# Performance work log

Measured on AMD Instinct MI355X. Metric: run time of the kernel, lower is better.

Reference implementation:

```python
import jax, jax.numpy as jnp
import numpy as np

B, T, H, L, V, M = 512, 64, 450, 56, 780, 8
S = T * B + 2  # slot 0 = zero padding vector, slots 1..T*B = edges, slot S-1 = dummy sink


def setup_inputs() -> dict:
    key = jax.random.key(0)
    ks = jax.random.split(key, 20)
    g = lambda i, shape, scale=0.05: jax.random.normal(ks[i], shape, jnp.float32) * scale
    return dict(
        tree_vecs=jax.random.normal(ks[0], (B, L), jnp.float32),
        x_wid=jax.random.randint(ks[1], (T, B), 0, V),
        pred_wid=jax.random.randint(ks[2], (T, B), 0, V),
        root_wid=jax.random.randint(ks[3], (B,), 0, V),
        h_nei_idx=jax.random.randint(ks[4], (T, B, M), 0, T * B + 1),
        o_nei_idx=jax.random.randint(ks[5], (T, B, M), 0, T * B + 1),
        root_o_nei_idx=jax.random.randint(ks[6], (B, M), 0, T * B + 1),
        valid=jax.random.randint(ks[7], (T, B), 0, 2),
        direction=jax.random.randint(ks[8], (T, B), 0, 2),
        emb=g(9, (V, H), 1.0),
        Wz=g(10, (H, 2 * H)), bz=jnp.zeros((H,), jnp.float32),
        Wr=g(11, (H, H)), br=jnp.zeros((H,), jnp.float32),
        Ur=g(12, (H, H)),
        Wh=g(13, (H, 2 * H)), bh=jnp.zeros((H,), jnp.float32),
        W=g(14, (H, L + H)), bW=jnp.zeros((H,), jnp.float32),
        U=g(15, (H, L + 2 * H)), bU=jnp.zeros((H,), jnp.float32),
        Wo=g(16, (V, H)), bWo=jnp.zeros((V,), jnp.float32),
        Us=g(17, (1, H)), bUs=jnp.zeros((1,), jnp.float32),
    )


def _gru(x, h_nei, Wz, bz, Wr, br, Ur, Wh, bh):
    # x: [N,H], h_nei: [N,M,H]  (JTNN tree GRU)
    sum_h = h_nei.sum(1)
    z = jax.nn.sigmoid(jnp.concatenate([x, sum_h], 1) @ Wz.T + bz)
    r = jax.nn.sigmoid((x @ Wr.T + br)[:, None, :] + h_nei @ Ur.T)
    gated = (r * h_nei).sum(1)
    h_tilde = jnp.tanh(jnp.concatenate([x, gated], 1) @ Wh.T + bh)
    return (1.0 - z) * sum_h + z * h_tilde


def reference(tree_vecs, x_wid, pred_wid, root_wid, h_nei_idx, o_nei_idx,
              root_o_nei_idx, valid, direction, emb, Wz, bz, Wr, br, Ur,
              Wh, bh, W, bW, U, bU, Wo, bWo, Us, bUs):
    xe_all = emb[x_wid]                              # [T,B,H]
    validf = valid.astype(jnp.float32)
    slots = jnp.arange(B)

    def step(h_buf, inputs):
        t, xe, h_idx, o_idx, v = inputs
        h_nei = h_buf[h_idx]                         # [B,M,H] gather (excl. real_y)
        new_h = _gru(xe, h_nei, Wz, bz, Wr, br, Ur, Wh, bh)
        cur_o = h_buf[o_idx].sum(1)                  # [B,H] sum-pool all neighbors
        slot = jnp.where(v > 0, 1 + t * B + slots, S - 1)
        h_buf = h_buf.at[slot].set(jnp.where(v[:, None] > 0, new_h, 0.0))
        return h_buf, (new_h, cur_o)

    h0 = jnp.zeros((S, H), jnp.float32)
    h_buf, (new_h_all, cur_o_all) = jax.lax.scan(
        step, h0, (jnp.arange(T), xe_all, h_nei_idx, o_nei_idx, valid))

    tv_rep = jnp.broadcast_to(tree_vecs, (T, B, L)).reshape(T * B, L)

    # ---- label (pred) loss: root rows + timestep rows where direction==1 ----
    pred_mask = jnp.concatenate([jnp.ones((B,), jnp.float32),
                                 (validf * direction.astype(jnp.float32)).reshape(-1)])
    pred_hidden = jnp.concatenate([jnp.zeros((B, H), jnp.float32),
                                   new_h_all.reshape(T * B, H)], 0)
    pred_tv = jnp.concatenate([tree_vecs, tv_rep], 0)
    pred_tgt = jnp.concatenate([root_wid, pred_wid.reshape(-1)])
    pv = jax.nn.relu(jnp.concatenate([pred_hidden, pred_tv], 1) @ W.T + bW)
    scores = pv @ Wo.T + bWo                         # [(T+1)*B, V]
    ll = jax.nn.log_softmax(scores, -1)
    ce = -jnp.take_along_axis(ll, pred_tgt[:, None], 1)[:, 0]
    pred_loss = (ce * pred_mask).sum() / B
    pred_acc = (((jnp.argmax(scores, 1) == pred_tgt).astype(jnp.float32)
                 * pred_mask).sum() / pred_mask.sum())

    # ---- topological (stop) loss: timestep rows + final root rows ----
    root_o = h_buf[root_o_nei_idx].sum(1)            # [B,H]
    stop_hidden = jnp.concatenate([
        jnp.concatenate([xe_all.reshape(T * B, H), cur_o_all.reshape(T * B, H), tv_rep], 1),
        jnp.concatenate([emb[root_wid], root_o, tree_vecs], 1)], 0)
    smask = jnp.concatenate([validf.reshape(-1), jnp.ones((B,), jnp.float32)])
    stgt = jnp.concatenate([direction.astype(jnp.float32).reshape(-1),
                            jnp.zeros((B,), jnp.float32)])
    sv = jax.nn.relu(stop_hidden @ U.T + bU)
    ss = (sv @ Us.T + bUs)[:, 0]
    bce = jnp.maximum(ss, 0.0) - ss * stgt + jnp.log1p(jnp.exp(-jnp.abs(ss)))
    stop_loss = (bce * smask).sum() / B
    stops = (ss >= 0).astype(jnp.float32)
    stop_acc = (((stops == stgt).astype(jnp.float32) * smask).sum() / smask.sum())

    return pred_loss, stop_loss, pred_acc, stop_acc
```

## Files before the change

### kernel.cpp

```cpp
#include <hip/hip_runtime.h>
#include <math.h>

#define Bq 512
#define Tq 64
#define Hq 450
#define Lq 56
#define Vq 780
#define Mq 8
#define TBq 32768
#define Sq 32770
#define HP 480
#define NPB 130
#define NPCAP 12288
#define NSCAP 20480
#define CH2 6144
#define NCH2 2

using bf16x8 = __attribute__((ext_vector_type(8))) __bf16;
using f32x4  = __attribute__((ext_vector_type(4))) float;
using u32x4  = __attribute__((ext_vector_type(4))) unsigned;

__device__ __forceinline__ ushort f2bf(float f){
    union { float f; unsigned u; } c; c.f = f;
    unsigned u = c.u;
    return (ushort)((u + 0x7FFFu + ((u >> 16) & 1u)) >> 16);
}
__device__ __forceinline__ float bf2f(ushort h){
    union { unsigned u; float f; } c; c.u = ((unsigned)h) << 16;
    return c.f;
}
__device__ __forceinline__ unsigned pk2(float a, float b){
    return (unsigned)f2bf(a) | ((unsigned)f2bf(b) << 16);
}
__device__ __forceinline__ float sigmf(float x){
    return __builtin_amdgcn_rcpf(1.f + __expf(-x));
}
__device__ __forceinline__ float tanhfast(float x){
    float e2 = __expf(2.f * x);
    return 1.f - 2.f * __builtin_amdgcn_rcpf(e2 + 1.f);
}

__global__ void convAll_k(
    const float* __restrict__ emb, const float* __restrict__ tree,
    const float* __restrict__ Wz, const float* __restrict__ Wr,
    const float* __restrict__ Ur, const float* __restrict__ Wh,
    const float* __restrict__ Wm, const float* __restrict__ U, const float* __restrict__ Wo,
    ushort* embb, ushort* treeb, ushort* WzX, ushort* WzS, ushort* WrB,
    ushort* WhX, ushort* WhG, ushort* UrB, ushort* WHp, ushort* UXp,
    ushort* UOp, ushort* WOp, ushort* WLp, ushort* ULp)
{
    int job = blockIdx.y, n = blockIdx.x;
    const float* src; ushort* dst; int Npad, Nsrc, Ksrc, Kpad, len, off;
    switch(job){
      case 0:  src=emb;  dst=embb; Npad=896; Nsrc=780; Ksrc=450; Kpad=480; len=450; off=0;   break;
      case 1:  src=tree; dst=treeb;Npad=512; Nsrc=512; Ksrc=56;  Kpad=64;  len=56;  off=0;   break;
      case 2:  src=Wz;   dst=WzX;  Npad=512; Nsrc=450; Ksrc=900; Kpad=480; len=450; off=0;   break;
      case 3:  src=Wz;   dst=WzS;  Npad=512; Nsrc=450; Ksrc=900; Kpad=480; len=450; off=450; break;
      case 4:  src=Wr;   dst=WrB;  Npad=512; Nsrc=450; Ksrc=450; Kpad=480; len=450; off=0;   break;
      case 5:  src=Wh;   dst=WhX;  Npad=512; Nsrc=450; Ksrc=900; Kpad=480; len=450; off=0;   break;
      case 6:  src=Wh;   dst=WhG;  Npad=512; Nsrc=450; Ksrc=900; Kpad=480; len=450; off=450; break;
      case 7:  src=Ur;   dst=UrB;  Npad=512; Nsrc=450; Ksrc=450; Kpad=480; len=450; off=0;   break;
      case 8:  src=Wm;   dst=WHp;  Npad=512; Nsrc=450; Ksrc=506; Kpad=480; len=450; off=0;   break;
      case 9:  src=U;    dst=UXp;  Npad=512; Nsrc=450; Ksrc=956; Kpad=480; len=450; off=0;   break;
      case 10: src=U;    dst=UOp;  Npad=512; Nsrc=450; Ksrc=956; Kpad=480; len=450; off=450; break;
      case 11: src=Wo;   dst=WOp;  Npad=832; Nsrc=780; Ksrc=450; Kpad=480; len=450; off=0;   break;
      case 12: src=Wm;   dst=WLp;  Npad=512; Nsrc=450; Ksrc=506; Kpad=64;  len=56;  off=450; break;
      default: src=U;    dst=ULp;  Npad=512; Nsrc=450; Ksrc=956; Kpad=64;  len=56;  off=900; break;
    }
    if (n >= Npad) return;
    for (int k = threadIdx.x; k < Kpad; k += blockDim.x){
        float v = 0.f;
        if (n < Nsrc && k < len) v = src[(size_t)n*Ksrc + off + k];
        dst[(size_t)n*Kpad + k] = f2bf(v);
    }
}

template<class APtr>
__device__ __forceinline__ void mgemm2(APtr&& aptr, const ushort* __restrict__ Bw, int ldb,
                                       int KT, int col0, f32x4 acc[4][2])
{
    __shared__ __align__(16) char As[2][128*80];
    __shared__ __align__(16) char Bs[2][64*80];
    const int tid = threadIdx.x;
    const int lane = tid & 63;
    const int w = tid >> 6, wm = w >> 1, wn = w & 1;
    const int ac = (tid & 3) * 8;
    const size_t boff = (size_t)(col0 + (tid >> 2)) * ldb;
    u32x4 ra0, ra1, rb;
    auto ld = [&](int k0){
        ra0 = *(const u32x4*)(aptr(0, k0) + ac);
        ra1 = *(const u32x4*)(aptr(1, k0) + ac);
        rb  = *(const u32x4*)(Bw + boff + k0 + ac);
    };
    const int wr_a0 = (tid>>2)*80 + (tid&3)*16;
    const int wr_a1 = ((tid>>2)+64)*80 + (tid&3)*16;
    const int wr_b  = (tid>>2)*80 + (tid&3)*16;
    const int rd_a  = (wm*64 + (lane&15))*80 + (lane>>4)*16;
    const int rd_b  = (wn*32 + (lane&15))*80 + (lane>>4)*16;
    ld(0);
    *(u32x4*)(As[0]+wr_a0) = ra0; *(u32x4*)(As[0]+wr_a1) = ra1; *(u32x4*)(Bs[0]+wr_b) = rb;
#pragma unroll
    for (int f=0;f<4;f++)
#pragma unroll
        for (int g=0;g<2;g++) acc[f][g] = (f32x4){0.f,0.f,0.f,0.f};
    __syncthreads();
    for (int kt=0; kt<KT; ++kt){
        const int cur = kt & 1;
        if (kt+1 < KT) ld((kt+1)*32);
        bf16x8 bF[2];
#pragma unroll
        for (int g=0; g<2; g++) bF[g] = *(const bf16x8*)(Bs[cur] + rd_b + g*16*80);
#pragma unroll
        for (int f=0; f<4; f++){
            bf16x8 aF = *(const bf16x8*)(As[cur] + rd_a + f*16*80);
#pragma unroll
            for (int g=0; g<2; g++)
                acc[f][g] = __builtin_amdgcn_mfma_f32_16x16x32_bf16(aF, bF[g], acc[f][g], 0, 0, 0);
        }
        if (kt+1 < KT){
            *(u32x4*)(As[cur^1]+wr_a0) = ra0; *(u32x4*)(As[cur^1]+wr_a1) = ra1;
            *(u32x4*)(Bs[cur^1]+wr_b) = rb;
        }
        __syncthreads();
    }
}

#define EPI_PRE  const int lane = threadIdx.x & 63; const int w_ = threadIdx.x >> 6; \
                 const int wm = w_ >> 1, wn = w_ & 1;

__device__ __forceinline__ void pre_body(const ushort* __restrict__ A, int lda,
    const ushort* __restrict__ Bw, const float* __restrict__ bias,
    ushort* __restrict__ out, int Mr, int KT)
{
    const int row0 = blockIdx.y*128, col0 = blockIdx.x*64;
    const int tid = threadIdx.x;
    const ushort* p0 = A + (size_t)(row0 + (tid>>2))*lda;
    const ushort* p1 = p0 + (size_t)64*lda;
    f32x4 acc[4][2];
    mgemm2([&](int which,int k0){ return (which?p1:p0)+k0; }, Bw, lda, KT, col0, acc);
    EPI_PRE
#pragma unroll
    for (int f=0; f<4; f++)
#pragma unroll
      for (int g=0; g<2; g++){
        int col = col0 + wn*32 + g*16 + (lane & 15);
        if (col >= HP) continue;
        float bb = 0.f;
        if (col < Hq && bias) bb = bias[col];
#pragma unroll
        for (int j=0; j<4; j++){
            int row = row0 + wm*64 + f*16 + ((lane>>4)<<2) + j;
            if (row < Mr) out[(size_t)row*HP + col] = (col < Hq) ? f2bf(acc[f][g][j] + bb) : 0;
        }
      }
}

__global__ __launch_bounds__(256) void preE_k(
    const ushort* __restrict__ embb,
    const ushort* __restrict__ WzX, const ushort* __restrict__ WrB,
    const ushort* __restrict__ WhX, const ushort* __restrict__ UXp,
    const float* __restrict__ bz, const float* __restrict__ br,
    const float* __restrict__ bh, const float* __restrict__ bU,
    ushort* __restrict__ EZ, ushort* __restrict__ ER,
    ushort* __restrict__ EH, ushort* __restrict__ EU)
{
    const ushort* Bw; const float* bias; ushort* out;
    switch(blockIdx.z){
      case 0:  Bw=WzX; bias=bz; out=EZ; break;
      case 1:  Bw=WrB; bias=br; out=ER; break;
      case 2:  Bw=WhX; bias=bh; out=EH; break;
      default: Bw=UXp; bias=bU; out=EU; break;
    }
    pre_body(embb, HP, Bw, bias, out, Vq, 15);
}

__global__ __launch_bounds__(256) void preT_k(
    const ushort* __restrict__ treeb,
    const ushort* __restrict__ WLp, const ushort* __restrict__ ULp,
    const float* __restrict__ bW, ushort* __restrict__ TP, ushort* __restrict__ TU)
{
    const ushort* Bw = blockIdx.z ? ULp : WLp;
    const float* bias = blockIdx.z ? nullptr : bW;
    ushort* out = blockIdx.z ? TU : TP;
    pre_body(treeb, 64, Bw, bias, out, Bq, 2);
}

__device__ __forceinline__ bool cmask(int which, int gr,
    const int* __restrict__ valid, const int* __restrict__ dir)
{
    if (which == 0) return (gr < Bq) ? true : (valid[gr-Bq] && dir[gr-Bq]);
    return (gr < TBq) ? (valid[gr] != 0) : true;
}
__global__ void cnt_k(const int* __restrict__ valid, const int* __restrict__ dir,
                      int* __restrict__ cnts)
{
    int which = blockIdx.y;
    int gr = blockIdx.x*256 + threadIdx.x;
    bool m = cmask(which, gr, valid, dir);
    unsigned long long bal = __ballot(m);
    if ((threadIdx.x & 63) == 0)
        atomicAdd(&cnts[which*NPB + blockIdx.x], (int)__popcll(bal));
}
__global__ void scan_k(const int* __restrict__ cnts, int* __restrict__ offs,
                       int* __restrict__ totals)
{
    if (threadIdx.x == 0){
        int a = 0;
        for (int i=0;i<NPB;i++){ offs[i] = a; a += cnts[i]; }
        totals[0] = a;
        int b = 0;
        for (int i=0;i<NPB;i++){ offs[NPB+i] = b; b += cnts[NPB+i]; }
        totals[1] = b;
    }
}
__global__ void fill_k(const int* __restrict__ valid, const int* __restrict__ dir,
                       const int* __restrict__ offs, int* __restrict__ listp,
                       int* __restrict__ lists)
{
    __shared__ int woff[4];
    int which = blockIdx.y;
    int gr = blockIdx.x*256 + threadIdx.x;
    bool m = cmask(which, gr, valid, dir);
    unsigned long long bal = __ballot(m);
    int lane = threadIdx.x & 63, wv = threadIdx.x >> 6;
    if (lane == 0) woff[wv] = (int)__popcll(bal);
    __syncthreads();
    int prev = 0;
    for (int i=0;i<wv;i++) prev += woff[i];
    if (m){
        int rank = prev + (int)__popcll(bal & ((1ull << lane) - 1ull));
        int pos = offs[which*NPB + blockIdx.x] + rank;
        if (which == 0){ if (pos < NPCAP) listp[pos] = gr; }
        else           { if (pos < NSCAP) lists[pos] = gr; }
    }
}

__global__ void vfill_k(const int* __restrict__ valid,
                        int* __restrict__ vcnt, int* __restrict__ vlist)
{
    __shared__ int woff[8];
    const int t = blockIdx.x;
    const int b = threadIdx.x;
    bool m = valid[t*Bq + b] != 0;
    unsigned long long bal = __ballot(m);
    int lane = b & 63, wv = b >> 6;
    if (lane == 0) woff[wv] = (int)__popcll(bal);
    __syncthreads();
    int prev = 0;
    for (int i=0;i<wv;i++) prev += woff[i];
    if (m) vlist[t*Bq + prev + (int)__popcll(bal & ((1ull<<lane)-1ull))] = b;
    if (threadIdx.x == 511){
        int tot = 0;
        for (int i=0;i<8;i++) tot += woff[i];
        vcnt[t] = tot;
    }
}

__global__ __launch_bounds__(256) void gather_k(int t,
    const int* __restrict__ x_wid, const int* __restrict__ h_nei_idx,
    const ushort* __restrict__ ER,
    const int* __restrict__ vcnt, const int* __restrict__ vlist,
    const ushort* __restrict__ hbuf, const ushort* __restrict__ uhbuf,
    ushort* __restrict__ sumhC, ushort* __restrict__ gatedC)
{
    const int cnt = vcnt[t];
    const int task = blockIdx.x*256 + threadIdx.x;
    if (task >= cnt*57) return;
    const int i = task / 57;
    const int c = task - i*57;
    const int j0 = c*8;
    const int b = vlist[t*Bq + i];
    const int base = t*Bq + b;
    const int wid = x_wid[base];
    const int* ip = h_nei_idx + (size_t)base*Mq;
    int idx[Mq];
#pragma unroll
    for (int m=0;m<Mq;m++) idx[m] = ip[m];
    float er[8];
    { u32x4 ev = *(const u32x4*)(ER + (size_t)wid*HP + j0);
#pragma unroll
      for (int e=0;e<8;e++) er[e] = bf2f((ushort)((ev[e>>1] >> ((e&1)*16)) & 0xffff)); }
    float sh[8] = {0,0,0,0,0,0,0,0};
    float gt[8] = {0,0,0,0,0,0,0,0};
#pragma unroll
    for (int m=0;m<Mq;m++){
        u32x4 hv = *(const u32x4*)(hbuf  + (size_t)idx[m]*HP + j0);
        u32x4 uv = *(const u32x4*)(uhbuf + (size_t)idx[m]*HP + j0);
#pragma unroll
        for (int e=0;e<8;e++){
            float h = bf2f((ushort)((hv[e>>1] >> ((e&1)*16)) & 0xffff));
            float u = bf2f((ushort)((uv[e>>1] >> ((e&1)*16)) & 0xffff));
            sh[e] += h;
            gt[e] += h * sigmf(er[e] + u);
        }
    }
    u32x4 so, go;
    so[0]=pk2(sh[0],sh[1]); so[1]=pk2(sh[2],sh[3]);
    so[2]=pk2(sh[4],sh[5]); so[3]=pk2(sh[6],sh[7]);
    go[0]=pk2(gt[0],gt[1]); go[1]=pk2(gt[2],gt[3]);
    go[2]=pk2(gt[4],gt[5]); go[3]=pk2(gt[6],gt[7]);
    *(u32x4*)(sumhC  + (size_t)i*HP + j0) = so;
    *(u32x4*)(gatedC + (size_t)i*HP + j0) = go;
}

__global__ __launch_bounds__(256) void zh_k(int t,
    const int* __restrict__ x_wid,
    const int* __restrict__ vcnt, const int* __restrict__ vlist,
    const ushort* __restrict__ EZ, const ushort* __restrict__ EH,
    const ushort* __restrict__ WzS, const ushort* __restrict__ WhG,
    const ushort* __restrict__ sumhC, const ushort* __restrict__ gatedC,
    ushort* __restrict__ nhC, ushort* __restrict__ hbuf)
{
    const int cnt = vcnt[t];
    const int rows0 = blockIdx.x*32;
    if (rows0 >= cnt) return;
    const int cols0 = blockIdx.y*32;
    const int lane = threadIdx.x & 63, w = threadIdx.x >> 6;
    const int wr = w >> 1, wc = w & 1;
    const int ai = rows0 + wr*16 + (lane & 15);
    const int C  = cols0 + wc*16 + (lane & 15);
    const int kq = (lane >> 4) * 8;
    const ushort* aZp = sumhC  + (size_t)ai*HP + kq;
    const ushort* aGp = gatedC + (size_t)ai*HP + kq;
    const ushort* bZp = WzS + (size_t)C*HP + kq;
    const ushort* bGp = WhG + (size_t)C*HP + kq;
    f32x4 accZ = (f32x4){0,0,0,0}, accH = (f32x4){0,0,0,0};
#pragma unroll 5
    for (int kt=0; kt<15; ++kt){
        const int kb = kt*32;
        bf16x8 aZ = *(const bf16x8*)(aZp + kb);
        bf16x8 aG = *(const bf16x8*)(aGp + kb);
        bf16x8 bZ = *(const bf16x8*)(bZp + kb);
        bf16x8 bG = *(const bf16x8*)(bGp + kb);
        accZ = __builtin_amdgcn_mfma_f32_16x16x32_bf16(aZ, bZ, accZ, 0, 0, 0);
        accH = __builtin_amdgcn_mfma_f32_16x16x32_bf16(aG, bG, accH, 0, 0, 0);
    }
#pragma unroll
    for (int j=0; j<4; j++){
        const int i = rows0 + wr*16 + ((lane>>4)<<2) + j;
        if (i >= cnt) continue;
        const int b = vlist[t*Bq + i];
        const int base = t*Bq + b;
        ushort o = 0;
        if (C < Hq){
            const int wid = x_wid[base];
            float z  = sigmf(accZ[j] + bf2f(EZ[(size_t)wid*HP + C]));
            float ht = tanhfast(accH[j] + bf2f(EH[(size_t)wid*HP + C]));
            float sh = bf2f(sumhC[(size_t)i*HP + C]);
            o = f2bf((1.f - z)*sh + z*ht);
            hbuf[(size_t)(1 + base)*HP + C] = o;
        }
        nhC[(size_t)i*HP + C] = o;
    }
}

__global__ __launch_bounds__(256) void ur_k(int t,
    const int* __restrict__ vcnt, const int* __restrict__ vlist,
    const ushort* __restrict__ UrB, const ushort* __restrict__ nhC,
    ushort* __restrict__ uhbuf)
{
    const int cnt = vcnt[t];
    const int rows0 = blockIdx.x*32;
    if (rows0 >= cnt) return;
    const int cols0 = blockIdx.y*32;
    const int lane = threadIdx.x & 63, w = threadIdx.x >> 6;
    const int wr = w >> 1, wc = w & 1;
    const int ai = rows0 + wr*16 + (lane & 15);
    const int C  = cols0 + wc*16 + (lane & 15);
    const int kq = (lane >> 4) * 8;
    const ushort* aNp = nhC + (size_t)ai*HP + kq;
    const ushort* bUp = UrB + (size_t)C*HP + kq;
    f32x4 acc = (f32x4){0,0,0,0};
#pragma unroll 5
    for (int kt=0; kt<15; ++kt){
        const int kb = kt*32;
        bf16x8 aN = *(const bf16x8*)(aNp + kb);
        bf16x8 bU = *(const bf16x8*)(bUp + kb);
        acc = __builtin_amdgcn_mfma_f32_16x16x32_bf16(aN, bU, acc, 0, 0, 0);
    }
    if (C < Hq){
#pragma unroll
        for (int j=0; j<4; j++){
            const int i = rows0 + wr*16 + ((lane>>4)<<2) + j;
            if (i >= cnt) continue;
            const int b = vlist[t*Bq + i];
            uhbuf[(size_t)(1 + t*Bq + b)*HP + C] = f2bf(acc[j]);
        }
    }
}

__global__ __launch_bounds__(256) void pred1c_k(const int* __restrict__ np_,
    const int* __restrict__ listp, const ushort* __restrict__ hbuf,
    const ushort* __restrict__ TP, const ushort* __restrict__ WHp,
    ushort* __restrict__ pv)
{
    const int np = *np_;
    const int row0 = blockIdx.x*128;
    if (row0 >= np) return;
    const int col0 = blockIdx.y*64;
    const int tid = threadIdx.x;
    int i0 = row0 + (tid>>2), i1 = i0 + 64;
    int g0 = (i0 < np) ? listp[i0] : 0;
    int g1 = (i1 < np) ? listp[i1] : 0;
    const ushort* p0 = (g0 < Bq) ? hbuf : hbuf + (size_t)(1 + g0 - Bq)*HP;
    const ushort* p1 = (g1 < Bq) ? hbuf : hbuf + (size_t)(1 + g1 - Bq)*HP;
    f32x4 acc[4][2];
    mgemm2([&](int which,int k0){ return (which?p1:p0)+k0; }, WHp, HP, 15, col0, acc);
    EPI_PRE
#pragma unroll
    for (int f=0; f<4; f++)
#pragma unroll
      for (int g=0; g<2; g++){
        int col = col0 + wn*32 + g*16 + (lane & 15);
        if (col >= HP) continue;
#pragma unroll
        for (int j=0; j<4; j++){
            int i = row0 + wm*64 + f*16 + ((lane>>4)<<2) + j;
            if (i >= np) continue;
            int gr = listp[i];
            int b = (gr < Bq) ? gr : ((gr - Bq) & (Bq-1));
            float v = 0.f;
            if (col < Hq) v = fmaxf(acc[f][g][j] + bf2f(TP[(size_t)b*HP + col]), 0.f);
            pv[(size_t)i*HP + col] = f2bf(v);
        }
      }
}

__global__ __launch_bounds__(256) void pred2c_k(int cs, const int* __restrict__ np_,
    const ushort* __restrict__ pv, const ushort* __restrict__ WOp,
    const float* __restrict__ bWo, float* __restrict__ scores)
{
    const int np = *np_;
    const int row0 = blockIdx.x*128;
    if (cs + row0 >= np) return;
    const int col0 = blockIdx.y*64;
    const int tid = threadIdx.x;
    const ushort* p0 = pv + (size_t)(cs + row0 + (tid>>2))*HP;
    const ushort* p1 = p0 + (size_t)64*HP;
    f32x4 acc[4][2];
    mgemm2([&](int which,int k0){ return (which?p1:p0)+k0; }, WOp, HP, 15, col0, acc);
    EPI_PRE
#pragma unroll
    for (int f=0; f<4; f++)
#pragma unroll
      for (int g=0; g<2; g++){
        int col = col0 + wn*32 + g*16 + (lane & 15);
        if (col >= Vq) continue;
        float bc = bWo[col];
#pragma unroll
        for (int j=0; j<4; j++){
            int r = row0 + wm*64 + f*16 + ((lane>>4)<<2) + j;
            scores[(size_t)r*832 + col] = acc[f][g][j] + bc;
        }
      }
}

__global__ __launch_bounds__(256) void predred_k(int cs, const int* __restrict__ np_,
    const int* __restrict__ listp, const float* __restrict__ scores,
    const int* __restrict__ pred_wid, const int* __restrict__ root_wid,
    float* __restrict__ accv)
{
    const int np = *np_;
    int nrows = np - cs; if (nrows > CH2) nrows = CH2;
    const int lane = threadIdx.x & 63, wv = threadIdx.x >> 6;
    const int wid_g = blockIdx.x*4 + wv, nw = gridDim.x*4;
    float ce = 0.f, hit = 0.f, cnt = 0.f;
    for (int r = wid_g; r < nrows; r += nw){
        const float* sc = scores + (size_t)r*832;
        int gr = listp[cs + r];
        int tgt = (gr < Bq) ? root_wid[gr] : pred_wid[gr - Bq];
        float vals[13];
        float bv = -INFINITY, tv = 0.f; int bi = 0;
#pragma unroll
        for (int q=0; q<13; q++){
            int j = lane + q*64;
            float v = (j < Vq) ? sc[j] : -INFINITY;
            vals[q] = v;
            if (v > bv){ bv = v; bi = j; }
            if (j == tgt) tv = v;
        }
#pragma unroll
        for (int off=32; off; off>>=1){
            float ov = __shfl_xor(bv, off); int oi = __shfl_xor(bi, off);
            if (ov > bv || (ov == bv && oi < bi)){ bv = ov; bi = oi; }
        }
        float s = 0.f;
#pragma unroll
        for (int q=0; q<13; q++){
            int j = lane + q*64;
            if (j < Vq) s += __expf(vals[q] - bv);
        }
#pragma unroll
        for (int off=32; off; off>>=1) s += __shfl_xor(s, off);
#pragma unroll
        for (int off=32; off; off>>=1) tv += __shfl_xor(tv, off);
        if (lane == 0){
            ce += bv + logf(s) - tv;
            hit += (bi == tgt) ? 1.f : 0.f;
            cnt += 1.f;
        }
    }
    __shared__ float L[3][4];
    if (lane == 0){ L[0][wv] = ce; L[1][wv] = hit; L[2][wv] = cnt; }
    __syncthreads();
    if (threadIdx.x == 0){
        float a = L[0][0]+L[0][1]+L[0][2]+L[0][3];
        float b = L[1][0]+L[1][1]+L[1][2]+L[1][3];
        float c = L[2][0]+L[2][1]+L[2][2]+L[2][3];
        if (c != 0.f){
            atomicAdd(&accv[0], a);
            atomicAdd(&accv[1], b);
            atomicAdd(&accv[2], c);
        }
    }
}

__global__ __launch_bounds__(256) void curo_c(const int* __restrict__ ns_,
    const int* __restrict__ lists,
    const int* __restrict__ o_nei_idx, const int* __restrict__ root_o_nei,
    const ushort* __restrict__ hbuf, ushort* __restrict__ curo)
{
    const int ns = *ns_;
    const int task = blockIdx.x*256 + threadIdx.x;
    if (task >= ns*60) return;
    const int i = task / 60;
    const int c = task - i*60;
    const int j0 = c*8;
    const int gr = lists[i];
    int idx[Mq];
    if (gr < TBq){
        int tt = gr >> 9;
#pragma unroll
        for (int m=0;m<Mq;m++){
            int ix = o_nei_idx[(size_t)gr*Mq + m];
            idx[m] = (ix <= tt*Bq) ? ix : 0;
        }
    } else {
#pragma unroll
        for (int m=0;m<Mq;m++) idx[m] = root_o_nei[(size_t)(gr-TBq)*Mq + m];
    }
    float sh[8] = {0,0,0,0,0,0,0,0};
#pragma unroll
    for (int m=0;m<Mq;m++){
        u32x4 hv = *(const u32x4*)(hbuf + (size_t)idx[m]*HP + j0);
#pragma unroll
        for (int e=0;e<8;e++)
            sh[e] += bf2f((ushort)((hv[e>>1] >> ((e&1)*16)) & 0xffff));
    }
    u32x4 so;
    so[0]=pk2(sh[0],sh[1]); so[1]=pk2(sh[2],sh[3]);
    so[2]=pk2(sh[4],sh[5]); so[3]=pk2(sh[6],sh[7]);
    *(u32x4*)(curo + (size_t)i*HP + j0) = so;
}

__global__ __launch_bounds__(256) void stopc_k(const int* __restrict__ ns_,
    const int* __restrict__ lists, const int* __restrict__ x_wid,
    const int* __restrict__ root_wid, const ushort* __restrict__ curo,
    const ushort* __restrict__ UOp, const ushort* __restrict__ EU,
    const ushort* __restrict__ TU, const float* __restrict__ Usf,
    float* __restrict__ ss)
{
    const int ns = *ns_;
    const int row0 = blockIdx.x*128;
    if (row0 >= ns) return;
    const int col0 = blockIdx.y*64;
    const int tid = threadIdx.x;
    const ushort* p0 = curo + (size_t)(row0 + (tid>>2))*HP;
    const ushort* p1 = p0 + (size_t)64*HP;
    f32x4 acc[4][2];
    mgemm2([&](int which,int k0){ return (which?p1:p0)+k0; }, UOp, HP, 15, col0, acc);
    EPI_PRE
#pragma unroll
    for (int f=0; f<4; f++){
#pragma unroll
        for (int j=0; j<4; j++){
            int i = row0 + wm*64 + f*16 + ((lane>>4)<<2) + j;
            float p = 0.f;
            if (i < ns){
                int gr = lists[i];
                int wid = (gr < TBq) ? x_wid[gr] : root_wid[gr - TBq];
                int b   = (gr < TBq) ? (gr & (Bq-1)) : (gr - TBq);
                const ushort* eu = EU + (size_t)wid*HP;
                const ushort* tu = TU + (size_t)b*HP;
#pragma unroll
                for (int g=0; g<2; g++){
                    int col = col0 + wn*32 + g*16 + (lane & 15);
                    if (col < Hq)
                        p += fmaxf(acc[f][g][j] + bf2f(eu[col]) + bf2f(tu[col]), 0.f) * Usf[col];
                }
            }
            p += __shfl_xor(p, 1); p += __shfl_xor(p, 2);
            p += __shfl_xor(p, 4); p += __shfl_xor(p, 8);
            if ((lane & 15) == 0 && i < ns) atomicAdd(&ss[i], p);
        }
    }
}

__global__ void stopfin_k(const int* __restrict__ ns_, const int* __restrict__ lists,
    const float* __restrict__ ss, const float* __restrict__ bUs,
    const int* __restrict__ direction, float* __restrict__ accv)
{
    const int ns = *ns_;
    int i = blockIdx.x*256 + threadIdx.x;
    float bce = 0.f, hit = 0.f, c = 0.f;
    if (i < ns){
        int gr = lists[i];
        float s = ss[i] + bUs[0];
        float stgt = (gr < TBq) ? (float)direction[gr] : 0.f;
        bce = fmaxf(s,0.f) - s*stgt + log1pf(__expf(-fabsf(s)));
        hit = ((((s >= 0.f) ? 1.f : 0.f) == stgt) ? 1.f : 0.f);
        c = 1.f;
    }
    for (int off=32; off; off>>=1){
        bce += __shfl_down(bce, off);
        hit += __shfl_down(hit, off);
        c   += __shfl_down(c,   off);
    }
    if ((threadIdx.x & 63) == 0 && c != 0.f){
        atomicAdd(&accv[3], bce);
        atomicAdd(&accv[4], hit);
        atomicAdd(&accv[5], c);
    }
}

__global__ void finalize_k(const float* __restrict__ accv, float* __restrict__ out){
    if (threadIdx.x == 0){
        out[0] = accv[0] / (float)Bq;
        out[1] = accv[3] / (float)Bq;
        out[2] = accv[1] / accv[2];
        out[3] = accv[4] / accv[5];
    }
}

extern "C" void kernel_launch(void* const* d_in, const int* in_sizes, int n_in,
                              void* d_out, int out_size, void* d_ws, size_t ws_size,
                              hipStream_t stream) {
    (void)in_sizes; (void)n_in; (void)out_size; (void)ws_size;
    const float* tree_vecs = (const float*)d_in[0];
    const int*   x_wid     = (const int*)d_in[1];
    const int*   pred_wid  = (const int*)d_in[2];
    const int*   root_wid  = (const int*)d_in[3];
    const int*   h_nei_idx = (const int*)d_in[4];
    const int*   o_nei_idx = (const int*)d_in[5];
    const int*   root_o_nei= (const int*)d_in[6];
    const int*   valid     = (const int*)d_in[7];
    const int*   direction = (const int*)d_in[8];
    const float* emb       = (const float*)d_in[9];
    const float* Wz        = (const float*)d_in[10];
    const float* bz        = (const float*)d_in[11];
    const float* Wr        = (const float*)d_in[12];
    const float* br        = (const float*)d_in[13];
    const float* Ur        = (const float*)d_in[14];
    const float* Wh        = (const float*)d_in[15];
    const float* bh        = (const float*)d_in[16];
    const float* Wm        = (const float*)d_in[17];
    const float* bW        = (const float*)d_in[18];
    const float* U         = (const float*)d_in[19];
    const float* bU        = (const float*)d_in[20];
    const float* Wo        = (const float*)d_in[21];
    const float* bWo       = (const float*)d_in[22];
    const float* Us        = (const float*)d_in[23];
    const float* bUs       = (const float*)d_in[24];

    char* w = (char*)d_ws; size_t off = 0;
    auto alloc = [&](size_t bytes)->void*{ void* p = w + off; off += (bytes + 255) & ~(size_t)255; return p; };

    ushort* hbuf  = (ushort*)alloc((size_t)Sq*HP*2);
    ushort* uhbuf = (ushort*)alloc((size_t)Sq*HP*2);
    ushort* embb  = (ushort*)alloc((size_t)896*HP*2);
    ushort* treeb = (ushort*)alloc((size_t)Bq*64*2);
    ushort* WzX   = (ushort*)alloc((size_t)512*HP*2);
    ushort* WzS   = (ushort*)alloc((size_t)512*HP*2);
    ushort* WrB   = (ushort*)alloc((size_t)512*HP*2);
    ushort* WhX   = (ushort*)alloc((size_t)512*HP*2);
    ushort* WhG   = (ushort*)alloc((size_t)512*HP*2);
    ushort* UrB   = (ushort*)alloc((size_t)512*HP*2);
    ushort* WHp   = (ushort*)alloc((size_t)512*HP*2);
    ushort* UXp   = (ushort*)alloc((size_t)512*HP*2);
    ushort* UOp   = (ushort*)alloc((size_t)512*HP*2);
    ushort* WOp   = (ushort*)alloc((size_t)832*HP*2);
    ushort* WLp   = (ushort*)alloc((size_t)512*64*2);
    ushort* ULp   = (ushort*)alloc((size_t)512*64*2);
    ushort* EZ    = (ushort*)alloc((size_t)896*HP*2);
    ushort* ER    = (ushort*)alloc((size_t)896*HP*2);
    ushort* EH    = (ushort*)alloc((size_t)896*HP*2);
    ushort* EU    = (ushort*)alloc((size_t)896*HP*2);
    ushort* TP    = (ushort*)alloc((size_t)Bq*HP*2);
    ushort* TU    = (ushort*)alloc((size_t)Bq*HP*2);
    ushort* sumhC = (ushort*)alloc((size_t)Bq*HP*2);
    ushort* gatedC= (ushort*)alloc((size_t)Bq*HP*2);
    ushort* nhC   = (ushort*)alloc((size_t)Bq*HP*2);
    ushort* pv    = (ushort*)alloc((size_t)NPCAP*HP*2);
    float*  scores= (float*)alloc((size_t)CH2*832*4);
    float*  ss    = (float*)alloc((size_t)NSCAP*4);
    int*    listp = (int*)alloc((size_t)NPCAP*4);
    int*    lists = (int*)alloc((size_t)NSCAP*4);
    int*    vlist = (int*)alloc((size_t)Tq*Bq*4);
    int*    vcnt  = (int*)alloc((size_t)Tq*4);
    int*    meta  = (int*)alloc((size_t)(NPB*4 + 2 + 16)*4);
    int*    cnts  = meta;
    int*    offs  = meta + 2*NPB;
    int*    tot   = meta + 4*NPB;
    float*  accv  = (float*)(meta + 4*NPB + 2);
    ushort* curo  = pv;

    (void)hipMemsetAsync(hbuf,  0, (size_t)Sq*HP*2, stream);
    (void)hipMemsetAsync(uhbuf, 0, (size_t)Sq*HP*2, stream);
    (void)hipMemsetAsync(ss,    0, (size_t)NSCAP*4, stream);
    (void)hipMemsetAsync(meta,  0, (size_t)(NPB*4 + 2 + 16)*4, stream);

    convAll_k<<<dim3(896,14), 128, 0, stream>>>(
        emb, tree_vecs, Wz, Wr, Ur, Wh, Wm, U, Wo,
        embb, treeb, WzX, WzS, WrB, WhX, WhG, UrB, WHp, UXp, UOp, WOp, WLp, ULp);

    preE_k<<<dim3(8,7,4), 256, 0, stream>>>(embb, WzX, WrB, WhX, UXp,
                                            bz, br, bh, bU, EZ, ER, EH, EU);
    preT_k<<<dim3(8,4,2), 256, 0, stream>>>(treeb, WLp, ULp, bW, TP, TU);

    cnt_k <<<dim3(NPB,2), 256, 0, stream>>>(valid, direction, cnts);
    scan_k<<<1, 64, 0, stream>>>(cnts, offs, tot);
    fill_k<<<dim3(NPB,2), 256, 0, stream>>>(valid, direction, offs, listp, lists);
    vfill_k<<<Tq, 512, 0, stream>>>(valid, vcnt, vlist);

    for (int t=0; t<Tq; t++){
        gather_k<<<115, 256, 0, stream>>>(t, x_wid, h_nei_idx, ER, vcnt, vlist,
                                          hbuf, uhbuf, sumhC, gatedC);
        zh_k<<<dim3(16,15), 256, 0, stream>>>(t, x_wid, vcnt, vlist, EZ, EH,
                                              WzS, WhG, sumhC, gatedC, nhC, hbuf);
        ur_k<<<dim3(16,15), 256, 0, stream>>>(t, vcnt, vlist, UrB, nhC, uhbuf);
    }

    pred1c_k<<<dim3(NPCAP/128, 8), 256, 0, stream>>>(tot, listp, hbuf, TP, WHp, pv);
    for (int c=0; c<NCH2; c++){
        int cs = c*CH2;
        pred2c_k<<<dim3(CH2/128, 13), 256, 0, stream>>>(cs, tot, pv, WOp, bWo, scores);
        predred_k<<<256, 256, 0, stream>>>(cs, tot, listp, scores, pred_wid, root_wid, accv);
    }

    curo_c<<<(NSCAP*60 + 255)/256, 256, 0, stream>>>(tot+1, lists, o_nei_idx, root_o_nei, hbuf, curo);
    stopc_k<<<dim3(NSCAP/128, 8), 256, 0, stream>>>(tot+1, lists, x_wid, root_wid,
                                                    curo, UOp, EU, TU, Us, ss);
    stopfin_k<<<NSCAP/256, 256, 0, stream>>>(tot+1, lists, ss, bUs, direction, accv);

    finalize_k<<<1, 64, 0, stream>>>(accv, (float*)d_out);
}
```

Baseline: 1.352 ms.

## Swap MFMA operands to transpose accumulators and vectorize GEMM epilogues

Swaps the A/B operands of the bf16 MFMA in the shared GEMM and in the per-step zh/ur kernels, so each lane holds four consecutive output columns of one row instead of four rows of one column. The epilogues of preE, zh, ur, pred1c, pred2c and stop now do 8- or 16-byte vector loads and stores per row and need fewer row-index lookups. The stop epilogue reduces across lane groups with fewer shuffles and issues one atomic per row. curo_c now writes zeros to the padding chunks directly instead of gathering them.

New measurement: 1.220 ms. -9.7%, faster.

```diff
diff --git a/kernel.cpp b/kernel.cpp
--- a/kernel.cpp
+++ b/kernel.cpp
@@ -115,7 +115,7 @@
             bf16x8 aF = *(const bf16x8*)(As[cur] + rd_a + f*16*80);
 #pragma unroll
             for (int g=0; g<2; g++)
-                acc[f][g] = __builtin_amdgcn_mfma_f32_16x16x32_bf16(aF, bF[g], acc[f][g], 0, 0, 0);
+                acc[f][g] = __builtin_amdgcn_mfma_f32_16x16x32_bf16(bF[g], aF, acc[f][g], 0, 0, 0);
         }
         if (kt+1 < KT){
             *(u32x4*)(As[cur^1]+wr_a0) = ra0; *(u32x4*)(As[cur^1]+wr_a1) = ra1;
@@ -140,19 +140,25 @@
     mgemm2([&](int which,int k0){ return (which?p1:p0)+k0; }, Bw, lda, KT, col0, acc);
     EPI_PRE
 #pragma unroll
-    for (int f=0; f<4; f++)
-#pragma unroll
-      for (int g=0; g<2; g++){
-        int col = col0 + wn*32 + g*16 + (lane & 15);
-        if (col >= HP) continue;
-        float bb = 0.f;
-        if (col < Hq && bias) bb = bias[col];
-#pragma unroll
-        for (int j=0; j<4; j++){
-            int row = row0 + wm*64 + f*16 + ((lane>>4)<<2) + j;
-            if (row < Mr) out[(size_t)row*HP + col] = (col < Hq) ? f2bf(acc[f][g][j] + bb) : 0;
-        }
-      }
+    for (int f=0; f<4; f++){
+        const int row = row0 + wm*64 + f*16 + (lane & 15);
+        if (row >= Mr) continue;
+#pragma unroll
+        for (int g=0; g<2; g++){
+            const int C4 = col0 + wn*32 + g*16 + ((lane>>4)<<2);
+            if (C4 >= HP) continue;
+            ushort o[4];
+#pragma unroll
+            for (int j=0; j<4; j++){
+                int col = C4 + j;
+                float bb = (col < Hq && bias) ? bias[col] : 0.f;
+                o[j] = (col < Hq) ? f2bf(acc[f][g][j] + bb) : 0;
+            }
+            uint2 ov; ov.x = (unsigned)o[0] | ((unsigned)o[1]<<16);
+            ov.y = (unsigned)o[2] | ((unsigned)o[3]<<16);
+            *(uint2*)(out + (size_t)row*HP + C4) = ov;
+        }
+    }
 }
 
 __global__ __launch_bounds__(256) void preE_k(
@@ -318,12 +324,12 @@
     const int lane = threadIdx.x & 63, w = threadIdx.x >> 6;
     const int wr = w >> 1, wc = w & 1;
     const int ai = rows0 + wr*16 + (lane & 15);
-    const int C  = cols0 + wc*16 + (lane & 15);
+    const int Cb = cols0 + wc*16 + (lane & 15);
     const int kq = (lane >> 4) * 8;
     const ushort* aZp = sumhC  + (size_t)ai*HP + kq;
     const ushort* aGp = gatedC + (size_t)ai*HP + kq;
-    const ushort* bZp = WzS + (size_t)C*HP + kq;
-    const ushort* bGp = WhG + (size_t)C*HP + kq;
+    const ushort* bZp = WzS + (size_t)Cb*HP + kq;
+    const ushort* bGp = WhG + (size_t)Cb*HP + kq;
     f32x4 accZ = (f32x4){0,0,0,0}, accH = (f32x4){0,0,0,0};
 #pragma unroll 5
     for (int kt=0; kt<15; ++kt){
@@ -332,25 +338,31 @@
         bf16x8 aG = *(const bf16x8*)(aGp + kb);
         bf16x8 bZ = *(const bf16x8*)(bZp + kb);
         bf16x8 bG = *(const bf16x8*)(bGp + kb);
-        accZ = __builtin_amdgcn_mfma_f32_16x16x32_bf16(aZ, bZ, accZ, 0, 0, 0);
-        accH = __builtin_amdgcn_mfma_f32_16x16x32_bf16(aG, bG, accH, 0, 0, 0);
-    }
-#pragma unroll
-    for (int j=0; j<4; j++){
-        const int i = rows0 + wr*16 + ((lane>>4)<<2) + j;
-        if (i >= cnt) continue;
-        const int b = vlist[t*Bq + i];
+        accZ = __builtin_amdgcn_mfma_f32_16x16x32_bf16(bZ, aZ, accZ, 0, 0, 0);
+        accH = __builtin_amdgcn_mfma_f32_16x16x32_bf16(bG, aG, accH, 0, 0, 0);
+    }
+    if (ai < cnt){
+        const int C4 = cols0 + wc*16 + ((lane>>4)<<2);
+        const int b = vlist[t*Bq + ai];
         const int base = t*Bq + b;
-        ushort o = 0;
-        if (C < Hq){
-            const int wid = x_wid[base];
-            float z  = sigmf(accZ[j] + bf2f(EZ[(size_t)wid*HP + C]));
-            float ht = tanhfast(accH[j] + bf2f(EH[(size_t)wid*HP + C]));
-            float sh = bf2f(sumhC[(size_t)i*HP + C]);
-            o = f2bf((1.f - z)*sh + z*ht);
-            hbuf[(size_t)(1 + base)*HP + C] = o;
-        }
-        nhC[(size_t)i*HP + C] = o;
+        const int wid = x_wid[base];
+        uint2 ez2 = *(const uint2*)(EZ + (size_t)wid*HP + C4);
+        uint2 eh2 = *(const uint2*)(EH + (size_t)wid*HP + C4);
+        uint2 sh2 = *(const uint2*)(sumhC + (size_t)ai*HP + C4);
+        unsigned ezw[2] = {ez2.x, ez2.y}, ehw[2] = {eh2.x, eh2.y}, shw[2] = {sh2.x, sh2.y};
+        ushort o[4];
+#pragma unroll
+        for (int j=0; j<4; j++){
+            const int C = C4 + j;
+            float z  = sigmf(accZ[j] + bf2f((ushort)((ezw[j>>1] >> ((j&1)*16)) & 0xffff)));
+            float ht = tanhfast(accH[j] + bf2f((ushort)((ehw[j>>1] >> ((j&1)*16)) & 0xffff)));
+            float sh = bf2f((ushort)((shw[j>>1] >> ((j&1)*16)) & 0xffff));
+            o[j] = (C < Hq) ? f2bf((1.f - z)*sh + z*ht) : 0;
+        }
+        uint2 ov; ov.x = (unsigned)o[0] | ((unsigned)o[1]<<16);
+        ov.y = (unsigned)o[2] | ((unsigned)o[3]<<16);
+        *(uint2*)(nhC + (size_t)ai*HP + C4) = ov;
+        *(uint2*)(hbuf + (size_t)(1 + base)*HP + C4) = ov;
     }
 }
 
@@ -366,26 +378,28 @@
     const int lane = threadIdx.x & 63, w = threadIdx.x >> 6;
     const int wr = w >> 1, wc = w & 1;
     const int ai = rows0 + wr*16 + (lane & 15);
-    const int C  = cols0 + wc*16 + (lane & 15);
+    const int Cb = cols0 + wc*16 + (lane & 15);
     const int kq = (lane >> 4) * 8;
     const ushort* aNp = nhC + (size_t)ai*HP + kq;
-    const ushort* bUp = UrB + (size_t)C*HP + kq;
+    const ushort* bUp = UrB + (size_t)Cb*HP + kq;
     f32x4 acc = (f32x4){0,0,0,0};
 #pragma unroll 5
     for (int kt=0; kt<15; ++kt){
         const int kb = kt*32;
         bf16x8 aN = *(const bf16x8*)(aNp + kb);
         bf16x8 bU = *(const bf16x8*)(bUp + kb);
-        acc = __builtin_amdgcn_mfma_f32_16x16x32_bf16(aN, bU, acc, 0, 0, 0);
-    }
-    if (C < Hq){
-#pragma unroll
-        for (int j=0; j<4; j++){
-            const int i = rows0 + wr*16 + ((lane>>4)<<2) + j;
-            if (i >= cnt) continue;
-            const int b = vlist[t*Bq + i];
-            uhbuf[(size_t)(1 + t*Bq + b)*HP + C] = f2bf(acc[j]);
-        }
+        acc = __builtin_amdgcn_mfma_f32_16x16x32_bf16(bU, aN, acc, 0, 0, 0);
+    }
+    if (ai < cnt){
+        const int C4 = cols0 + wc*16 + ((lane>>4)<<2);
+        const int b = vlist[t*Bq + ai];
+        ushort o[4];
+#pragma unroll
+        for (int j=0; j<4; j++)
+            o[j] = (C4 + j < Hq) ? f2bf(acc[j]) : 0;
+        uint2 ov; ov.x = (unsigned)o[0] | ((unsigned)o[1]<<16);
+        ov.y = (unsigned)o[2] | ((unsigned)o[3]<<16);
+        *(uint2*)(uhbuf + (size_t)(1 + t*Bq + b)*HP + C4) = ov;
     }
 }
 
@@ -408,22 +422,28 @@
     mgemm2([&](int which,int k0){ return (which?p1:p0)+k0; }, WHp, HP, 15, col0, acc);
     EPI_PRE
 #pragma unroll
-    for (int f=0; f<4; f++)
-#pragma unroll
-      for (int g=0; g<2; g++){
-        int col = col0 + wn*32 + g*16 + (lane & 15);
-        if (col >= HP) continue;
-#pragma unroll
-        for (int j=0; j<4; j++){
-            int i = row0 + wm*64 + f*16 + ((lane>>4)<<2) + j;
-            if (i >= np) continue;
-            int gr = listp[i];
-            int b = (gr < Bq) ? gr : ((gr - Bq) & (Bq-1));
-            float v = 0.f;
-            if (col < Hq) v = fmaxf(acc[f][g][j] + bf2f(TP[(size_t)b*HP + col]), 0.f);
-            pv[(size_t)i*HP + col] = f2bf(v);
-        }
-      }
+    for (int f=0; f<4; f++){
+        const int i = row0 + wm*64 + f*16 + (lane & 15);
+        if (i >= np) continue;
+        const int gr = listp[i];
+        const int b = (gr < Bq) ? gr : ((gr - Bq) & (Bq-1));
+#pragma unroll
+        for (int g=0; g<2; g++){
+            const int C4 = col0 + wn*32 + g*16 + ((lane>>4)<<2);
+            if (C4 >= HP) continue;
+            uint2 tp2 = *(const uint2*)(TP + (size_t)b*HP + C4);
+            unsigned tpw[2] = {tp2.x, tp2.y};
+            ushort o[4];
+#pragma unroll
+            for (int j=0; j<4; j++){
+                float v = fmaxf(acc[f][g][j] + bf2f((ushort)((tpw[j>>1] >> ((j&1)*16)) & 0xffff)), 0.f);
+                o[j] = f2bf(v);
+            }
+            uint2 ov; ov.x = (unsigned)o[0] | ((unsigned)o[1]<<16);
+            ov.y = (unsigned)o[2] | ((unsigned)o[3]<<16);
+            *(uint2*)(pv + (size_t)i*HP + C4) = ov;
+        }
+    }
 }
 
 __global__ __launch_bounds__(256) void pred2c_k(int cs, const int* __restrict__ np_,
@@ -441,18 +461,21 @@
     mgemm2([&](int which,int k0){ return (which?p1:p0)+k0; }, WOp, HP, 15, col0, acc);
     EPI_PRE
 #pragma unroll
-    for (int f=0; f<4; f++)
-#pragma unroll
-      for (int g=0; g<2; g++){
-        int col = col0 + wn*32 + g*16 + (lane & 15);
-        if (col >= Vq) continue;
-        float bc = bWo[col];
-#pragma unroll
-        for (int j=0; j<4; j++){
-            int r = row0 + wm*64 + f*16 + ((lane>>4)<<2) + j;
-            scores[(size_t)r*832 + col] = acc[f][g][j] + bc;
-        }
-      }
+    for (int f=0; f<4; f++){
+        const int r = row0 + wm*64 + f*16 + (lane & 15);
+#pragma unroll
+        for (int g=0; g<2; g++){
+            const int C4 = col0 + wn*32 + g*16 + ((lane>>4)<<2);
+            float4 ov;
+            float* op = (float*)&ov;
+#pragma unroll
+            for (int j=0; j<4; j++){
+                int col = C4 + j;
+                op[j] = acc[f][g][j] + ((col < Vq) ? bWo[col] : 0.f);
+            }
+            *(float4*)(scores + (size_t)r*832 + C4) = ov;
+        }
+    }
 }
 
 __global__ __launch_bounds__(256) void predred_k(int cs, const int* __restrict__ np_,
@@ -526,6 +549,11 @@
     const int i = task / 60;
     const int c = task - i*60;
     const int j0 = c*8;
+    if (c >= 57){
+        u32x4 z = (u32x4){0,0,0,0};
+        *(u32x4*)(curo + (size_t)i*HP + j0) = z;
+        return;
+    }
     const int gr = lists[i];
     int idx[Mq];
     if (gr < TBq){
@@ -572,27 +600,32 @@
     EPI_PRE
 #pragma unroll
     for (int f=0; f<4; f++){
-#pragma unroll
-        for (int j=0; j<4; j++){
-            int i = row0 + wm*64 + f*16 + ((lane>>4)<<2) + j;
-            float p = 0.f;
-            if (i < ns){
-                int gr = lists[i];
-                int wid = (gr < TBq) ? x_wid[gr] : root_wid[gr - TBq];
-                int b   = (gr < TBq) ? (gr & (Bq-1)) : (gr - TBq);
-                const ushort* eu = EU + (size_t)wid*HP;
-                const ushort* tu = TU + (size_t)b*HP;
-#pragma unroll
-                for (int g=0; g<2; g++){
-                    int col = col0 + wn*32 + g*16 + (lane & 15);
-                    if (col < Hq)
-                        p += fmaxf(acc[f][g][j] + bf2f(eu[col]) + bf2f(tu[col]), 0.f) * Usf[col];
+        const int i = row0 + wm*64 + f*16 + (lane & 15);
+        float p = 0.f;
+        if (i < ns){
+            const int gr = lists[i];
+            const int wid = (gr < TBq) ? x_wid[gr] : root_wid[gr - TBq];
+            const int b   = (gr < TBq) ? (gr & (Bq-1)) : (gr - TBq);
+#pragma unroll
+            for (int g=0; g<2; g++){
+                const int C4 = col0 + wn*32 + g*16 + ((lane>>4)<<2);
+                if (C4 >= Hq) continue;
+                uint2 eu2 = *(const uint2*)(EU + (size_t)wid*HP + C4);
+                uint2 tu2 = *(const uint2*)(TU + (size_t)b*HP + C4);
+                unsigned euw[2] = {eu2.x, eu2.y}, tuw[2] = {tu2.x, tu2.y};
+#pragma unroll
+                for (int j=0; j<4; j++){
+                    const int col = C4 + j;
+                    if (col < Hq){
+                        float e = bf2f((ushort)((euw[j>>1] >> ((j&1)*16)) & 0xffff));
+                        float u = bf2f((ushort)((tuw[j>>1] >> ((j&1)*16)) & 0xffff));
+                        p += fmaxf(acc[f][g][j] + e + u, 0.f) * Usf[col];
+                    }
                 }
             }
-            p += __shfl_xor(p, 1); p += __shfl_xor(p, 2);
-            p += __shfl_xor(p, 4); p += __shfl_xor(p, 8);
-            if ((lane & 15) == 0 && i < ns) atomicAdd(&ss[i], p);
-        }
+        }
+        p += __shfl_xor(p, 16); p += __shfl_xor(p, 32);
+        if ((lane >> 4) == 0 && i < ns) atomicAdd(&ss[i], p);
     }
 }
 
```
